# Kernel optimization log

Measured on AMD Instinct MI355X. Metric: run time of the kernel, lower is better.

Reference implementation:

```python
import jax, jax.numpy as jnp
import numpy as np

IN_DIM, UNITS, OUT_DIM = 128, 256, 8
DENSITY = 0.5  # 1 - sparsity_level
B, T = 256, 512


def _ncp_dims():
    Nm = OUT_DIM
    Nc = max(int(0.4 * (UNITS - Nm)), 1)   # command neurons (AutoNCP rule)
    Ni = UNITS - Nm - Nc                    # inter neurons
    return Ni, Nc, Nm


def _fanout_mask(rng, n_src, n_dst, fanout):
    # each source connects to `fanout` distinct random destinations
    idx = np.argsort(rng.random((n_src, n_dst)), axis=1)[:, :fanout]
    m = np.zeros((n_src, n_dst), dtype=np.int32)
    m[np.arange(n_src)[:, None], idx] = 1
    return m


def setup_inputs() -> dict:
    key = jax.random.key(0)
    rng = np.random.default_rng(22222)
    Ni, Nc, Nm = _ncp_dims()
    s_fan = max(int(Ni * DENSITY), 1)       # sensory fanout
    i_fan = max(int(Nc * DENSITY), 1)       # inter fanout
    m_fanin = max(int(Nc * DENSITY), 1)     # motor fanin
    M_si = _fanout_mask(rng, IN_DIM, Ni, s_fan)      # sensory -> inter
    M_ic = _fanout_mask(rng, Ni, Nc, i_fan)          # inter -> command
    M_cm = _fanout_mask(rng, Nm, Nc, m_fanin).T      # command -> motor (fanin per motor)

    def layer_mask(M_in, hid):
        # WiredCfCCell: concat input sparsity with dense ones for the recurrent block, then transpose
        return np.concatenate([M_in, np.ones((hid, hid), np.int32)], axis=0).T

    masks = [layer_mask(M_si, Ni), layer_mask(M_ic, Nc), layer_mask(M_cm, Nm)]
    dims = [(IN_DIM, Ni), (Ni, Nc), (Nc, Nm)]
    inp = {}
    for l, (fin, hid) in enumerate(dims):
        cat = fin + hid
        scale = 1.0 / np.sqrt(cat)
        for nm in ("w1", "w2", "wa", "wb"):
            inp[f"{nm}_{l}"] = jnp.asarray(rng.normal(0.0, scale, (hid, cat)).astype(np.float32))
        for nm in ("b1", "b2", "ba", "bb"):
            inp[f"{nm}_{l}"] = jnp.zeros((hid,), jnp.float32)
        inp[f"m{l}"] = jnp.asarray(masks[l])  # int32, constant sparsity mask
    k1, k2 = jax.random.split(key)
    inp["x"] = jax.random.normal(k1, (B, T, IN_DIM), jnp.float32)
    inp["dt"] = jax.random.uniform(k2, (1,), jnp.float32, 0.5, 1.5)
    return inp


def _cfc_cell(xh, w1, b1, w2, b2, wa, ba, wb, bb, m, ts):
    # CfCCell, mode='default', no backbone, sparsity mask on ff1/ff2 weights
    mf = m.astype(w1.dtype)
    ff1 = jnp.tanh(xh @ (w1 * mf).T + b1)
    ff2 = jnp.tanh(xh @ (w2 * mf).T + b2)
    t_interp = jax.nn.sigmoid((xh @ wa.T + ba) * ts + (xh @ wb.T + bb))
    return ff1 * (1.0 - t_interp) + t_interp * ff2


def _forward(x, dt, params, masks):
    Ni, Nc, Nm = _ncp_dims()
    ts = dt[0]
    h0 = jnp.zeros((x.shape[0], Ni), x.dtype)
    h1 = jnp.zeros((x.shape[0], Nc), x.dtype)
    h2 = jnp.zeros((x.shape[0], Nm), x.dtype)
    p0, p1, p2 = params

    def step(carry, xt):
        h0, h1, h2 = carry
        nh0 = _cfc_cell(jnp.concatenate([xt, h0], 1), *p0, masks[0], ts)
        nh1 = _cfc_cell(jnp.concatenate([nh0, h1], 1), *p1, masks[1], ts)
        nh2 = _cfc_cell(jnp.concatenate([nh1, h2], 1), *p2, masks[2], ts)
        return (nh0, nh1, nh2), nh2

    (h0, h1, h2), ys = jax.lax.scan(step, (h0, h1, h2), jnp.swapaxes(x, 0, 1))
    y = jnp.tanh(jnp.swapaxes(ys, 0, 1))          # (B, T, OUT_DIM), tanh output saturation
    h_out = jnp.concatenate([h0, h1, h2], axis=1)  # (B, units)
    return y, h_out


def reference(x, dt,
              w1_0, b1_0, w2_0, b2_0, wa_0, ba_0, wb_0, bb_0, m0,
              w1_1, b1_1, w2_1, b2_1, wa_1, ba_1, wb_1, bb_1, m1,
              w1_2, b1_2, w2_2, b2_2, wa_2, ba_2, wb_2, bb_2, m2):
    params = ((w1_0, b1_0, w2_0, b2_0, wa_0, ba_0, wb_0, bb_0),
              (w1_1, b1_1, w2_1, b2_1, wa_1, ba_1, wb_1, bb_1),
              (w1_2, b1_2, w2_2, b2_2, wa_2, ba_2, wb_2, bb_2))
    return _forward(x, dt, params, (m0, m1, m2))
```

## Files before the change

kernel.cpp:

```cpp
#include <hip/hip_runtime.h>
#include <cmath>


typedef _Float16 f16;
typedef f16 h4 __attribute__((ext_vector_type(4)));
typedef f16 h8 __attribute__((ext_vector_type(8)));
typedef float f4 __attribute__((ext_vector_type(4)));

#define MFMA(a, b, c) __builtin_amdgcn_mfma_f32_16x16x32_f16(a, b, c, 0, 0, 0)
#define RAW_BAR() asm volatile("s_waitcnt lgkmcnt(0)\n\ts_barrier" ::: "memory")

constexpr int IN_DIM = 128, Ni = 149, Nc = 99, Nm = 8;
constexpr int CAT0 = 277, CAT1 = 248, CAT2 = 107;
constexpr int Bsz = 256, Tsz = 512;
constexpr int TC = 128, NCH = 4, NBT = 16;
constexpr int NT0 = 30, NT1 = 21;
constexpr int S0 = 168, S2 = 136;
constexpr size_t XU0_HALVES = (size_t)TC * NBT * NT0 * 256;
constexpr size_t NH0_HALVES = (size_t)TC * NBT * 16 * 160;
constexpr size_t XU1_HALVES = (size_t)TC * NBT * NT1 * 256;
constexpr size_t H0S_HALVES = (size_t)NBT * 16 * S0;
constexpr size_t H12S_HALVES = (size_t)NBT * 2 * 16 * S2;
constexpr size_t YOFF = (size_t)Bsz * Tsz * 8;

constexpr int OFF_X0 = 0;
constexpr int OFF_R0 = 7680;
constexpr int OFF_X1 = 17280;
constexpr int OFF_R12A = 24000;
constexpr int OFF_R12B = 29376;
constexpr int NFRAG = 30144;

__device__ inline float rcpf_(float x) { return __builtin_amdgcn_rcpf(x); }
__device__ __forceinline__ float cfc_h(float a0, float a1, float a2) {
  float e0 = __expf(a0), e1 = __expf(a1), e2 = __expf(a2);
  float pa = 1.f + e0, ma = 1.f - e0;
  float pb = 1.f + e1, mb = 1.f - e1;
  float pc = 1.f + e2;
  float num = fmaf(ma * pb, e2, mb * pa);
  return num * rcpf_(pa * pb * pc);
}
__device__ __forceinline__ float tanhp_(float x) {
  float e = __expf(-2.f * x);
  return (1.f - e) * rcpf_(1.f + e);
}

__global__ __launch_bounds__(256) void pack_kernel(
    const float* __restrict__ w1_0, const float* __restrict__ w2_0,
    const float* __restrict__ wa_0, const float* __restrict__ wb_0,
    const int* __restrict__ m0,
    const float* __restrict__ w1_1, const float* __restrict__ w2_1,
    const float* __restrict__ wa_1, const float* __restrict__ wb_1,
    const int* __restrict__ m1,
    const float* __restrict__ w1_2, const float* __restrict__ w2_2,
    const float* __restrict__ wa_2, const float* __restrict__ wb_2,
    const int* __restrict__ m2, const float* __restrict__ dtp,
    f16* __restrict__ PK) {
  int idx = blockIdx.x * 256 + threadIdx.x;
  if (idx >= NFRAG) return;
  int lane = idx & 63, col = lane & 15, q = lane >> 4;
  float ts = dtp[0];
  const float* Wa = nullptr;
  const float* Wb = nullptr;
  const int* M = nullptr;
  int ld, n, nmax, k0, kmax;
  int mat;
  if (idx < OFF_R0) {
    int p = idx >> 6;
    mat = p / 40; int nt = (p >> 2) % 10, kt = p & 3;
    ld = CAT0; n = nt * 16 + col; nmax = Ni; k0 = kt * 32 + q * 8; kmax = IN_DIM;
    if (mat == 0) { Wa = w1_0; M = m0; }
    else if (mat == 1) { Wa = w2_0; M = m0; }
    else { Wa = wa_0; Wb = wb_0; }
  } else if (idx < OFF_X1) {
    int p = (idx - OFF_R0) >> 6;
    int g = p / 15; mat = (p / 5) % 3; int kt = p % 5;
    ld = CAT0; n = g * 16 + col; nmax = Ni; k0 = IN_DIM + kt * 32 + q * 8; kmax = CAT0;
    if (mat == 0) Wa = w1_0;
    else if (mat == 1) Wa = w2_0;
    else { Wa = wa_0; Wb = wb_0; }
  } else if (idx < OFF_R12A) {
    int p = (idx - OFF_X1) >> 6;
    mat = p / 35; int nt = (p / 5) % 7, kt = p % 5;
    ld = CAT1; n = nt * 16 + col; nmax = Nc; k0 = kt * 32 + q * 8; kmax = Ni;
    if (mat == 0) { Wa = w1_1; M = m1; }
    else if (mat == 1) { Wa = w2_1; M = m1; }
    else { Wa = wa_1; Wb = wb_1; }
  } else if (idx < OFF_R12B) {
    int p = (idx - OFF_R12A) >> 6;
    int wv = p / 12; mat = (p / 4) % 3; int kt = p & 3;
    ld = CAT1; n = wv * 16 + col; nmax = Nc; k0 = Ni + kt * 32 + q * 8; kmax = CAT1;
    if (mat == 0) Wa = w1_1;
    else if (mat == 1) Wa = w2_1;
    else { Wa = wa_1; Wb = wb_1; }
  } else {
    int p = (idx - OFF_R12B) >> 6;
    mat = p / 4; int kt = p & 3;
    ld = CAT2; n = col; nmax = Nm; k0 = kt * 32 + q * 8; kmax = CAT2;
    if (mat == 0) { Wa = w1_2; M = m2; }
    else if (mat == 1) { Wa = w2_2; M = m2; }
    else { Wa = wa_2; Wb = wb_2; }
  }
  h8 r;
#pragma unroll
  for (int j = 0; j < 8; j++) {
    int k = k0 + j;
    float v = 0.f;
    if (n < nmax && k < kmax) {
      if (mat < 2) {
        v = Wa[(size_t)n * ld + k];
        if (M) v *= (float)M[(size_t)n * ld + k];
        v *= -2.f;
      } else {
        v = -(ts * Wa[(size_t)n * ld + k] + Wb[(size_t)n * ld + k]);
      }
    }
    r[j] = (f16)v;
  }
  ((h8*)PK)[idx] = r;
}

__global__ __launch_bounds__(192, 2) void X_kernel(
    const h8* __restrict__ pk, const float* __restrict__ x,
    const f16* __restrict__ NH0, f16* __restrict__ XU0, f16* __restrict__ XU1,
    const float* __restrict__ b1_0, const float* __restrict__ b2_0,
    const float* __restrict__ ba_0, const float* __restrict__ bb_0,
    const float* __restrict__ b1_1, const float* __restrict__ b2_1,
    const float* __restrict__ ba_1, const float* __restrict__ bb_1,
    const float* __restrict__ dtp, int c) {
  __shared__ f16 stg[16 * 136];
  int tid = threadIdx.x;
  int w = tid >> 6, lane = tid & 63, col = lane & 15, q = lane >> 4;
  int wg = blockIdx.x;
  float ts = dtp[0];
  if (wg < 512) {
    if (c < 0) return;
    h8 Bf[7][5];
    float bias[7];
#pragma unroll
    for (int nt = 0; nt < 7; nt++) {
#pragma unroll
      for (int kt = 0; kt < 5; kt++)
        Bf[nt][kt] = pk[OFF_X1 + ((w * 7 + nt) * 5 + kt) * 64 + lane];
      int n = nt * 16 + col;
      bias[nt] = (n < Nc) ? (w == 0 ? -2.f * b1_1[n]
                                    : (w == 1 ? -2.f * b2_1[n]
                                              : -(ts * ba_1[n] + bb_1[n])))
                          : 0.f;
    }
    for (int i = 0; i < 4; i++) {
      int mt = wg * 4 + i;
      const f16* Ab = NH0 + (size_t)mt * 2560;
      h8 A[5];
#pragma unroll
      for (int kt = 0; kt < 5; kt++)
        A[kt] = *(const h8*)(Ab + col * 160 + kt * 32 + q * 8);
#pragma unroll
      for (int nt = 0; nt < 7; nt++) {
        float b = bias[nt];
        f4 acc = {b, b, b, b};
#pragma unroll
        for (int kt = 0; kt < 5; kt++) acc = MFMA(A[kt], Bf[nt][kt], acc);
        h4 o;
#pragma unroll
        for (int rr = 0; rr < 4; rr++) o[rr] = (f16)acc[rr];
        *(h4*)(XU1 + ((size_t)mt * NT1 + w * 7 + nt) * 256 + lane * 4) = o;
      }
    }
  } else {
    int cn = c + 1;
    if (cn >= NCH) return;
    int bx = wg - 512;
    h8 Bf[10][4];
    float bias[10];
#pragma unroll
    for (int nt = 0; nt < 10; nt++) {
#pragma unroll
      for (int kt = 0; kt < 4; kt++)
        Bf[nt][kt] = pk[OFF_X0 + ((w * 10 + nt) * 4 + kt) * 64 + lane];
      int n = nt * 16 + col;
      bias[nt] = (n < Ni) ? (w == 0 ? -2.f * b1_0[n]
                                    : (w == 1 ? -2.f * b2_0[n]
                                              : -(ts * ba_0[n] + bb_0[n])))
                          : 0.f;
    }
    for (int i = 0; i < 4; i++) {
      int mt = bx * 4 + i;
      int tl = mt >> 4, bt = mt & 15;
      int tg = cn * TC + tl;
      if (tid < 128) {
        int sr = tid >> 3, sc = (tid & 7) * 16;
        const float* xp = x + ((size_t)(bt * 16 + sr) * Tsz + tg) * IN_DIM + sc;
        h8 hv0, hv1;
#pragma unroll
        for (int j = 0; j < 8; j++) hv0[j] = (f16)xp[j];
#pragma unroll
        for (int j = 0; j < 8; j++) hv1[j] = (f16)xp[8 + j];
        *(h8*)(stg + sr * 136 + sc) = hv0;
        *(h8*)(stg + sr * 136 + sc + 8) = hv1;
      }
      __syncthreads();
      h8 A[4];
#pragma unroll
      for (int kt = 0; kt < 4; kt++)
        A[kt] = *(const h8*)(stg + col * 136 + kt * 32 + q * 8);
#pragma unroll
      for (int nt = 0; nt < 10; nt++) {
        float b = bias[nt];
        f4 acc = {b, b, b, b};
#pragma unroll
        for (int kt = 0; kt < 4; kt++) acc = MFMA(A[kt], Bf[nt][kt], acc);
        h4 o;
#pragma unroll
        for (int rr = 0; rr < 4; rr++) o[rr] = (f16)acc[rr];
        *(h4*)(XU0 + ((size_t)mt * NT0 + w * 10 + nt) * 256 + lane * 4) = o;
      }
      __syncthreads();
    }
  }
}

__device__ __forceinline__ void r0_step(
    const f16* br, f16* bw, const f16* __restrict__ XU0, f16* __restrict__ NH0,
    float* __restrict__ out, const h8 (&Bf)[3][5], h4 (&xu)[3],
    int t, int tload, int bt, int g, int lane, int col, int q, int n, bool last) {
  h8 A[5];
#pragma unroll
  for (int kt = 0; kt < 5; kt++)
    A[kt] = *(const h8*)(br + col * S0 + kt * 32 + q * 8);
  f4 acc0 = {(float)xu[0][0], (float)xu[0][1], (float)xu[0][2], (float)xu[0][3]};
  f4 acc1 = {(float)xu[1][0], (float)xu[1][1], (float)xu[1][2], (float)xu[1][3]};
  f4 acc2 = {(float)xu[2][0], (float)xu[2][1], (float)xu[2][2], (float)xu[2][3]};
  size_t mtl = (size_t)tload * NBT + bt;
#pragma unroll
  for (int mat = 0; mat < 3; mat++)
    xu[mat] = *(const h4*)(XU0 + (mtl * NT0 + mat * 10 + g) * 256 + lane * 4);
#pragma unroll
  for (int kt = 0; kt < 5; kt++) {
    acc0 = MFMA(A[kt], Bf[0][kt], acc0);
    acc1 = MFMA(A[kt], Bf[1][kt], acc1);
    acc2 = MFMA(A[kt], Bf[2][kt], acc2);
  }
  int mt = t * NBT + bt;
  f16* nh = NH0 + (size_t)mt * 2560;
#pragma unroll
  for (int r = 0; r < 4; r++) {
    int m = q * 4 + r;
    float h = cfc_h(acc0[r], acc1[r], acc2[r]);
    f16 h16 = (f16)h;
    bw[m * S0 + n] = h16;
    nh[m * 160 + n] = h16;
    if (last && n < Ni) out[YOFF + (size_t)(bt * 16 + m) * 256 + n] = h;
  }
}

__device__ __forceinline__ void r12l1_step(
    const f16* br, f16* bw, const f16* __restrict__ XU1, float* __restrict__ out,
    const h8 (&Bf)[3][4], h4 (&xu)[3],
    int tload, int bt, int w, int lane, int col, int q, int n, bool last) {
  h8 A[4];
#pragma unroll
  for (int kt = 0; kt < 4; kt++)
    A[kt] = *(const h8*)(br + col * S2 + kt * 32 + q * 8);
  f4 acc0 = {(float)xu[0][0], (float)xu[0][1], (float)xu[0][2], (float)xu[0][3]};
  f4 acc1 = {(float)xu[1][0], (float)xu[1][1], (float)xu[1][2], (float)xu[1][3]};
  f4 acc2 = {(float)xu[2][0], (float)xu[2][1], (float)xu[2][2], (float)xu[2][3]};
  size_t mtl = (size_t)tload * NBT + bt;
#pragma unroll
  for (int mat = 0; mat < 3; mat++)
    xu[mat] = *(const h4*)(XU1 + (mtl * NT1 + mat * 7 + w) * 256 + lane * 4);
#pragma unroll
  for (int kt = 0; kt < 4; kt++) {
    acc0 = MFMA(A[kt], Bf[0][kt], acc0);
    acc1 = MFMA(A[kt], Bf[1][kt], acc1);
    acc2 = MFMA(A[kt], Bf[2][kt], acc2);
  }
#pragma unroll
  for (int r = 0; r < 4; r++) {
    int m = q * 4 + r;
    float h = cfc_h(acc0[r], acc1[r], acc2[r]);
    if (n < Nc) {
      bw[m * S2 + n] = (f16)h;
      if (last) out[YOFF + (size_t)(bt * 16 + m) * 256 + Ni + n] = h;
    }
  }
}

__device__ __forceinline__ void r12l2_step(
    const f16* rb, f16* wb, float* __restrict__ out, const h8 (&Bf)[3][4],
    float bn0, float bn1, float bn2, int tg, int bt, int col, int q, bool last) {
  h8 A[4];
#pragma unroll
  for (int kt = 0; kt < 4; kt++)
    A[kt] = *(const h8*)(rb + col * S2 + kt * 32 + q * 8);
  f4 acc0 = {bn0, bn0, bn0, bn0};
  f4 acc1 = {bn1, bn1, bn1, bn1};
  f4 acc2 = {bn2, bn2, bn2, bn2};
#pragma unroll
  for (int kt = 0; kt < 4; kt++) {
    acc0 = MFMA(A[kt], Bf[0][kt], acc0);
    acc1 = MFMA(A[kt], Bf[1][kt], acc1);
    acc2 = MFMA(A[kt], Bf[2][kt], acc2);
  }
#pragma unroll
  for (int r = 0; r < 4; r++) {
    int m = q * 4 + r;
    float h = cfc_h(acc0[r], acc1[r], acc2[r]);
    if (col < Nm) {
      out[((size_t)(bt * 16 + m) * Tsz + tg) * 8 + col] = tanhp_(h);
      wb[m * S2 + Nc + col] = (f16)h;
      if (last) out[YOFF + (size_t)(bt * 16 + m) * 256 + Ni + Nc + col] = h;
    }
  }
}

__global__ __launch_bounds__(640) void R_kernel(
    const h8* __restrict__ pk,
    const float* __restrict__ c1, const float* __restrict__ c2,
    const float* __restrict__ ca, const float* __restrict__ cb,
    const float* __restrict__ dtp, const f16* __restrict__ XU0,
    const f16* __restrict__ XU1, f16* __restrict__ NH0,
    f16* __restrict__ H0S, f16* __restrict__ H12S, float* __restrict__ out, int c) {
  __shared__ __align__(16) char smem[2 * 16 * S0 * 2];
  int tid = threadIdx.x;
  int g = tid >> 6, lane = tid & 63, col = lane & 15, q = lane >> 4;
  int wg = blockIdx.x;

  if (wg < NBT) {
    if (c >= NCH) return;
    f16(*buf)[16 * S0] = (f16(*)[16 * S0])smem;
    int bt = wg;
    int n = g * 16 + col;
    h8 Bf[3][5];
#pragma unroll
    for (int mat = 0; mat < 3; mat++)
#pragma unroll
      for (int kt = 0; kt < 5; kt++)
        Bf[mat][kt] = pk[OFF_R0 + ((g * 3 + mat) * 5 + kt) * 64 + lane];

    for (int idx = tid; idx < 16 * S0; idx += 640) {
      buf[0][idx] = (c == 0) ? (f16)0.f : H0S[(size_t)bt * 16 * S0 + idx];
      buf[1][idx] = (f16)0.f;
    }
    __syncthreads();

    h4 xuA[3], xuB[3];
#pragma unroll
    for (int mat = 0; mat < 3; mat++) {
      xuA[mat] = *(const h4*)(XU0 + ((size_t)bt * NT0 + mat * 10 + g) * 256 + lane * 4);
      xuB[mat] =
          *(const h4*)(XU0 + ((size_t)(NBT + bt) * NT0 + mat * 10 + g) * 256 + lane * 4);
    }

    for (int t = 0; t < TC; t += 2) {
      bool lastA = (c == NCH - 1) && (t == TC - 1);
      int tlA = (t + 2 < TC) ? t + 2 : t;
      r0_step(buf[0], buf[1], XU0, NH0, out, Bf, xuA, t, tlA, bt, g, lane, col, q, n,
              lastA);
      RAW_BAR();
      bool lastB = (c == NCH - 1) && (t + 1 == TC - 1);
      int tlB = (t + 3 < TC) ? t + 3 : t + 1;
      r0_step(buf[1], buf[0], XU0, NH0, out, Bf, xuB, t + 1, tlB, bt, g, lane, col, q,
              n, lastB);
      RAW_BAR();
    }
    for (int idx = tid; idx < 16 * S0; idx += 640)
      H0S[(size_t)bt * 16 * S0 + idx] = buf[0][idx];

  } else {
    int cc = c - 1;
    if (cc < 0) return;
    f16(*buf)[16 * S2] = (f16(*)[16 * S2])smem;
    int bt = wg - NBT;
    int w = g;
    float ts = dtp[0];
    h8 Bf[3][4];
    float bn0 = 0.f, bn1 = 0.f, bn2 = 0.f;
    int n = w * 16 + col;
    if (w < 7) {
#pragma unroll
      for (int mat = 0; mat < 3; mat++)
#pragma unroll
        for (int kt = 0; kt < 4; kt++)
          Bf[mat][kt] = pk[OFF_R12A + ((w * 3 + mat) * 4 + kt) * 64 + lane];
    } else if (w == 7) {
#pragma unroll
      for (int mat = 0; mat < 3; mat++)
#pragma unroll
        for (int kt = 0; kt < 4; kt++)
          Bf[mat][kt] = pk[OFF_R12B + (mat * 4 + kt) * 64 + lane];
      bn0 = (col < Nm) ? -2.f * c1[col] : 0.f;
      bn1 = (col < Nm) ? -2.f * c2[col] : 0.f;
      bn2 = (col < Nm) ? -(ts * ca[col] + cb[col]) : 0.f;
    }
    for (int idx = tid; idx < 2 * 16 * S2; idx += 640)
      ((f16*)buf)[idx] = (cc == 0) ? (f16)0.f : H12S[(size_t)bt * 2 * 16 * S2 + idx];
    __syncthreads();

    h4 xuA[3], xuB[3];
    if (w < 7) {
#pragma unroll
      for (int mat = 0; mat < 3; mat++) {
        xuA[mat] =
            *(const h4*)(XU1 + ((size_t)bt * NT1 + mat * 7 + w) * 256 + lane * 4);
        xuB[mat] = *(const h4*)(XU1 +
                                ((size_t)(NBT + bt) * NT1 + mat * 7 + w) * 256 +
                                lane * 4);
      }
    }

    for (int t = 0; t < TC; t += 2) {
      if (w < 7) {
        int tlA = (t + 2 < TC) ? t + 2 : t;
        bool lastA = (cc == NCH - 1) && (t == TC - 1);
        r12l1_step(buf[0], buf[1], XU1, out, Bf, xuA, tlA, bt, w, lane, col, q, n,
                   lastA);
      }
      RAW_BAR();
      if (w == 7)
        r12l2_step(buf[1], buf[0], out, Bf, bn0, bn1, bn2, cc * TC + t, bt, col, q,
                   false);
      if (w < 7) {
        int tlB = (t + 3 < TC) ? t + 3 : t + 1;
        bool lastB = (cc == NCH - 1) && (t + 1 == TC - 1);
        r12l1_step(buf[1], buf[0], XU1, out, Bf, xuB, tlB, bt, w, lane, col, q, n,
                   lastB);
      }
      RAW_BAR();
      if (w == 7)
        r12l2_step(buf[0], buf[1], out, Bf, bn0, bn1, bn2, cc * TC + t + 1, bt, col, q,
                   (cc == NCH - 1) && (t + 1 == TC - 1));
    }
    __syncthreads();
    for (int idx = tid; idx < 2 * 16 * S2; idx += 640)
      H12S[(size_t)bt * 2 * 16 * S2 + idx] = ((f16*)buf)[idx];
  }
}

extern "C" void kernel_launch(void* const* d_in, const int* in_sizes, int n_in,
                              void* d_out, int out_size, void* d_ws, size_t ws_size,
                              hipStream_t stream) {
  const float* w1_0 = (const float*)d_in[0];
  const float* w2_0 = (const float*)d_in[1];
  const float* wa_0 = (const float*)d_in[2];
  const float* wb_0 = (const float*)d_in[3];
  const float* b1_0 = (const float*)d_in[4];
  const float* b2_0 = (const float*)d_in[5];
  const float* ba_0 = (const float*)d_in[6];
  const float* bb_0 = (const float*)d_in[7];
  const int* m0 = (const int*)d_in[8];
  const float* w1_1 = (const float*)d_in[9];
  const float* w2_1 = (const float*)d_in[10];
  const float* wa_1 = (const float*)d_in[11];
  const float* wb_1 = (const float*)d_in[12];
  const float* b1_1 = (const float*)d_in[13];
  const float* b2_1 = (const float*)d_in[14];
  const float* ba_1 = (const float*)d_in[15];
  const float* bb_1 = (const float*)d_in[16];
  const int* m1 = (const int*)d_in[17];
  const float* w1_2 = (const float*)d_in[18];
  const float* w2_2 = (const float*)d_in[19];
  const float* wa_2 = (const float*)d_in[20];
  const float* wb_2 = (const float*)d_in[21];
  const float* c1 = (const float*)d_in[22];
  const float* c2 = (const float*)d_in[23];
  const float* ca = (const float*)d_in[24];
  const float* cb = (const float*)d_in[25];
  const int* m2 = (const int*)d_in[26];
  const float* x = (const float*)d_in[27];
  const float* dt = (const float*)d_in[28];
  float* out = (float*)d_out;

  f16* XU0 = (f16*)d_ws;
  f16* NH0 = XU0 + XU0_HALVES;
  f16* XU1 = NH0 + NH0_HALVES;
  f16* H0S = XU1 + XU1_HALVES;
  f16* H12S = H0S + H0S_HALVES;
  f16* PK = H12S + H12S_HALVES;
  const h8* pk = (const h8*)PK;

  pack_kernel<<<(NFRAG + 255) / 256, 256, 0, stream>>>(
      w1_0, w2_0, wa_0, wb_0, m0, w1_1, w2_1, wa_1, wb_1, m1,
      w1_2, w2_2, wa_2, wb_2, m2, dt, PK);

  X_kernel<<<1024, 192, 0, stream>>>(pk, x, NH0, XU0, XU1, b1_0, b2_0, ba_0, bb_0,
                                     b1_1, b2_1, ba_1, bb_1, dt, -1);

  for (int c = 0; c <= NCH; c++) {
    R_kernel<<<32, 640, 0, stream>>>(pk, c1, c2, ca, cb, dt, XU0, XU1, NH0, H0S,
                                     H12S, out, c);
    if (c < NCH)
      X_kernel<<<1024, 192, 0, stream>>>(pk, x, NH0, XU0, XU1, b1_0, b2_0, ba_0,
                                         bb_0, b1_1, b2_1, ba_1, bb_1, dt, c);
  }
}
```

Baseline: 828.4 us.

## Fuse input projection into recurrent kernel and compute layer-1 input on the fly

Removes the separate X_kernel launches. The layer-0 input projection now runs on extra workgroups inside R_kernel, concurrently with the recurrences, using double-buffered XU0 and NH0 chunks. The layer-1 input projection is no longer precomputed into XU1: the layer-1 waves multiply directly against NH0 tiles that are staged into LDS by two extra prefetch waves. The chunk size is halved to 64 timesteps, which doubles the number of chunks and launches. This trades extra MFMA work on the serial recurrent critical path for fewer launches, less memory traffic and overlap of the projection with the recurrence.

```diff
diff --git a/kernel.cpp b/kernel.cpp
--- a/kernel.cpp
+++ b/kernel.cpp
@@ -13,12 +13,12 @@
 constexpr int IN_DIM = 128, Ni = 149, Nc = 99, Nm = 8;
 constexpr int CAT0 = 277, CAT1 = 248, CAT2 = 107;
 constexpr int Bsz = 256, Tsz = 512;
-constexpr int TC = 128, NCH = 4, NBT = 16;
-constexpr int NT0 = 30, NT1 = 21;
+constexpr int TC = 64, NCH = 8, NBT = 16;
+constexpr int NT0 = 30;
 constexpr int S0 = 168, S2 = 136;
-constexpr size_t XU0_HALVES = (size_t)TC * NBT * NT0 * 256;
-constexpr size_t NH0_HALVES = (size_t)TC * NBT * 16 * 160;
-constexpr size_t XU1_HALVES = (size_t)TC * NBT * NT1 * 256;
+constexpr int NXWG = 128;
+constexpr size_t XU0C = (size_t)TC * NBT * NT0 * 256;
+constexpr size_t NH0C = (size_t)TC * NBT * 2560;
 constexpr size_t H0S_HALVES = (size_t)NBT * 16 * S0;
 constexpr size_t H12S_HALVES = (size_t)NBT * 2 * 16 * S2;
 constexpr size_t YOFF = (size_t)Bsz * Tsz * 8;
@@ -119,106 +119,6 @@
   ((h8*)PK)[idx] = r;
 }
 
-__global__ __launch_bounds__(192, 2) void X_kernel(
-    const h8* __restrict__ pk, const float* __restrict__ x,
-    const f16* __restrict__ NH0, f16* __restrict__ XU0, f16* __restrict__ XU1,
-    const float* __restrict__ b1_0, const float* __restrict__ b2_0,
-    const float* __restrict__ ba_0, const float* __restrict__ bb_0,
-    const float* __restrict__ b1_1, const float* __restrict__ b2_1,
-    const float* __restrict__ ba_1, const float* __restrict__ bb_1,
-    const float* __restrict__ dtp, int c) {
-  __shared__ f16 stg[16 * 136];
-  int tid = threadIdx.x;
-  int w = tid >> 6, lane = tid & 63, col = lane & 15, q = lane >> 4;
-  int wg = blockIdx.x;
-  float ts = dtp[0];
-  if (wg < 512) {
-    if (c < 0) return;
-    h8 Bf[7][5];
-    float bias[7];
-#pragma unroll
-    for (int nt = 0; nt < 7; nt++) {
-#pragma unroll
-      for (int kt = 0; kt < 5; kt++)
-        Bf[nt][kt] = pk[OFF_X1 + ((w * 7 + nt) * 5 + kt) * 64 + lane];
-      int n = nt * 16 + col;
-      bias[nt] = (n < Nc) ? (w == 0 ? -2.f * b1_1[n]
-                                    : (w == 1 ? -2.f * b2_1[n]
-                                              : -(ts * ba_1[n] + bb_1[n])))
-                          : 0.f;
-    }
-    for (int i = 0; i < 4; i++) {
-      int mt = wg * 4 + i;
-      const f16* Ab = NH0 + (size_t)mt * 2560;
-      h8 A[5];
-#pragma unroll
-      for (int kt = 0; kt < 5; kt++)
-        A[kt] = *(const h8*)(Ab + col * 160 + kt * 32 + q * 8);
-#pragma unroll
-      for (int nt = 0; nt < 7; nt++) {
-        float b = bias[nt];
-        f4 acc = {b, b, b, b};
-#pragma unroll
-        for (int kt = 0; kt < 5; kt++) acc = MFMA(A[kt], Bf[nt][kt], acc);
-        h4 o;
-#pragma unroll
-        for (int rr = 0; rr < 4; rr++) o[rr] = (f16)acc[rr];
-        *(h4*)(XU1 + ((size_t)mt * NT1 + w * 7 + nt) * 256 + lane * 4) = o;
-      }
-    }
-  } else {
-    int cn = c + 1;
-    if (cn >= NCH) return;
-    int bx = wg - 512;
-    h8 Bf[10][4];
-    float bias[10];
-#pragma unroll
-    for (int nt = 0; nt < 10; nt++) {
-#pragma unroll
-      for (int kt = 0; kt < 4; kt++)
-        Bf[nt][kt] = pk[OFF_X0 + ((w * 10 + nt) * 4 + kt) * 64 + lane];
-      int n = nt * 16 + col;
-      bias[nt] = (n < Ni) ? (w == 0 ? -2.f * b1_0[n]
-                                    : (w == 1 ? -2.f * b2_0[n]
-                                              : -(ts * ba_0[n] + bb_0[n])))
-                          : 0.f;
-    }
-    for (int i = 0; i < 4; i++) {
-      int mt = bx * 4 + i;
-      int tl = mt >> 4, bt = mt & 15;
-      int tg = cn * TC + tl;
-      if (tid < 128) {
-        int sr = tid >> 3, sc = (tid & 7) * 16;
-        const float* xp = x + ((size_t)(bt * 16 + sr) * Tsz + tg) * IN_DIM + sc;
-        h8 hv0, hv1;
-#pragma unroll
-        for (int j = 0; j < 8; j++) hv0[j] = (f16)xp[j];
-#pragma unroll
-        for (int j = 0; j < 8; j++) hv1[j] = (f16)xp[8 + j];
-        *(h8*)(stg + sr * 136 + sc) = hv0;
-        *(h8*)(stg + sr * 136 + sc + 8) = hv1;
-      }
-      __syncthreads();
-      h8 A[4];
-#pragma unroll
-      for (int kt = 0; kt < 4; kt++)
-        A[kt] = *(const h8*)(stg + col * 136 + kt * 32 + q * 8);
-#pragma unroll
-      for (int nt = 0; nt < 10; nt++) {
-        float b = bias[nt];
-        f4 acc = {b, b, b, b};
-#pragma unroll
-        for (int kt = 0; kt < 4; kt++) acc = MFMA(A[kt], Bf[nt][kt], acc);
-        h4 o;
-#pragma unroll
-        for (int rr = 0; rr < 4; rr++) o[rr] = (f16)acc[rr];
-        *(h4*)(XU0 + ((size_t)mt * NT0 + w * 10 + nt) * 256 + lane * 4) = o;
-      }
-      __syncthreads();
-    }
-  }
-}
-
 __device__ __forceinline__ void r0_step(
     const f16* br, f16* bw, const f16* __restrict__ XU0, f16* __restrict__ NH0,
     float* __restrict__ out, const h8 (&Bf)[3][5], h4 (&xu)[3],
@@ -254,25 +154,26 @@
 }
 
 __device__ __forceinline__ void r12l1_step(
-    const f16* br, f16* bw, const f16* __restrict__ XU1, float* __restrict__ out,
-    const h8 (&Bf)[3][4], h4 (&xu)[3],
-    int tload, int bt, int w, int lane, int col, int q, int n, bool last) {
-  h8 A[4];
-#pragma unroll
-  for (int kt = 0; kt < 4; kt++)
-    A[kt] = *(const h8*)(br + col * S2 + kt * 32 + q * 8);
-  f4 acc0 = {(float)xu[0][0], (float)xu[0][1], (float)xu[0][2], (float)xu[0][3]};
-  f4 acc1 = {(float)xu[1][0], (float)xu[1][1], (float)xu[1][2], (float)xu[1][3]};
-  f4 acc2 = {(float)xu[2][0], (float)xu[2][1], (float)xu[2][2], (float)xu[2][3]};
-  size_t mtl = (size_t)tload * NBT + bt;
-#pragma unroll
-  for (int mat = 0; mat < 3; mat++)
-    xu[mat] = *(const h4*)(XU1 + (mtl * NT1 + mat * 7 + w) * 256 + lane * 4);
+    const f16* brN, const f16* br, f16* bw, float* __restrict__ out,
+    const h8 (&BfI)[3][5], const h8 (&BfR)[3][4],
+    float bn0, float bn1, float bn2,
+    int bt, int col, int q, int n, bool last) {
+  f4 acc0 = {bn0, bn0, bn0, bn0};
+  f4 acc1 = {bn1, bn1, bn1, bn1};
+  f4 acc2 = {bn2, bn2, bn2, bn2};
+#pragma unroll
+  for (int kt = 0; kt < 5; kt++) {
+    h8 A = *(const h8*)(brN + col * S0 + kt * 32 + q * 8);
+    acc0 = MFMA(A, BfI[0][kt], acc0);
+    acc1 = MFMA(A, BfI[1][kt], acc1);
+    acc2 = MFMA(A, BfI[2][kt], acc2);
+  }
 #pragma unroll
   for (int kt = 0; kt < 4; kt++) {
-    acc0 = MFMA(A[kt], Bf[0][kt], acc0);
-    acc1 = MFMA(A[kt], Bf[1][kt], acc1);
-    acc2 = MFMA(A[kt], Bf[2][kt], acc2);
+    h8 A = *(const h8*)(br + col * S2 + kt * 32 + q * 8);
+    acc0 = MFMA(A, BfR[0][kt], acc0);
+    acc1 = MFMA(A, BfR[1][kt], acc1);
+    acc2 = MFMA(A, BfR[2][kt], acc2);
   }
 #pragma unroll
   for (int r = 0; r < 4; r++) {
@@ -315,18 +216,26 @@
 
 __global__ __launch_bounds__(640) void R_kernel(
     const h8* __restrict__ pk,
+    const float* __restrict__ b1_0, const float* __restrict__ b2_0,
+    const float* __restrict__ ba_0, const float* __restrict__ bb_0,
+    const float* __restrict__ b1_1, const float* __restrict__ b2_1,
+    const float* __restrict__ ba_1, const float* __restrict__ bb_1,
     const float* __restrict__ c1, const float* __restrict__ c2,
     const float* __restrict__ ca, const float* __restrict__ cb,
-    const float* __restrict__ dtp, const f16* __restrict__ XU0,
-    const f16* __restrict__ XU1, f16* __restrict__ NH0,
-    f16* __restrict__ H0S, f16* __restrict__ H12S, float* __restrict__ out, int c) {
-  __shared__ __align__(16) char smem[2 * 16 * S0 * 2];
+    const float* __restrict__ dtp, const float* __restrict__ x,
+    f16* __restrict__ XU0, f16* __restrict__ NH0,
+    f16* __restrict__ H0S, f16* __restrict__ H12S,
+    float* __restrict__ out, int c) {
+  __shared__ __align__(16) char smem[19456];
   int tid = threadIdx.x;
   int g = tid >> 6, lane = tid & 63, col = lane & 15, q = lane >> 4;
   int wg = blockIdx.x;
+  float ts = dtp[0];
 
   if (wg < NBT) {
-    if (c >= NCH) return;
+    if (c < 0 || c >= NCH) return;
+    const f16* XU0r = XU0 + (size_t)(c & 1) * XU0C;
+    f16* NH0w = NH0 + (size_t)(c & 1) * NH0C;
     f16(*buf)[16 * S0] = (f16(*)[16 * S0])smem;
     int bt = wg;
     int n = g * 16 + col;
@@ -346,93 +255,172 @@
     h4 xuA[3], xuB[3];
 #pragma unroll
     for (int mat = 0; mat < 3; mat++) {
-      xuA[mat] = *(const h4*)(XU0 + ((size_t)bt * NT0 + mat * 10 + g) * 256 + lane * 4);
-      xuB[mat] =
-          *(const h4*)(XU0 + ((size_t)(NBT + bt) * NT0 + mat * 10 + g) * 256 + lane * 4);
+      xuA[mat] = *(const h4*)(XU0r + ((size_t)bt * NT0 + mat * 10 + g) * 256 + lane * 4);
+      xuB[mat] = *(const h4*)(XU0r +
+                              ((size_t)(NBT + bt) * NT0 + mat * 10 + g) * 256 + lane * 4);
     }
 
     for (int t = 0; t < TC; t += 2) {
-      bool lastA = (c == NCH - 1) && (t == TC - 1);
       int tlA = (t + 2 < TC) ? t + 2 : t;
-      r0_step(buf[0], buf[1], XU0, NH0, out, Bf, xuA, t, tlA, bt, g, lane, col, q, n,
-              lastA);
+      r0_step(buf[0], buf[1], XU0r, NH0w, out, Bf, xuA, t, tlA, bt, g, lane, col, q, n,
+              false);
       RAW_BAR();
       bool lastB = (c == NCH - 1) && (t + 1 == TC - 1);
       int tlB = (t + 3 < TC) ? t + 3 : t + 1;
-      r0_step(buf[1], buf[0], XU0, NH0, out, Bf, xuB, t + 1, tlB, bt, g, lane, col, q,
+      r0_step(buf[1], buf[0], XU0r, NH0w, out, Bf, xuB, t + 1, tlB, bt, g, lane, col, q,
               n, lastB);
       RAW_BAR();
     }
     for (int idx = tid; idx < 16 * S0; idx += 640)
       H0S[(size_t)bt * 16 * S0 + idx] = buf[0][idx];
 
-  } else {
+  } else if (wg < 2 * NBT) {
     int cc = c - 1;
-    if (cc < 0) return;
+    if (cc < 0 || cc >= NCH) return;
+    const f16* NH0r = NH0 + (size_t)(cc & 1) * NH0C;
     f16(*buf)[16 * S2] = (f16(*)[16 * S2])smem;
+    f16* bufN0 = (f16*)(smem + 2 * 16 * S2 * 2);
+    f16* bufN1 = bufN0 + 16 * S0;
     int bt = wg - NBT;
     int w = g;
-    float ts = dtp[0];
-    h8 Bf[3][4];
+    int n = w * 16 + col;
+    h8 BfI[3][5], BfR[3][4], Bf2[3][4];
     float bn0 = 0.f, bn1 = 0.f, bn2 = 0.f;
-    int n = w * 16 + col;
     if (w < 7) {
 #pragma unroll
+      for (int mat = 0; mat < 3; mat++) {
+#pragma unroll
+        for (int kt = 0; kt < 5; kt++)
+          BfI[mat][kt] = pk[OFF_X1 + (mat * 35 + w * 5 + kt) * 64 + lane];
+#pragma unroll
+        for (int kt = 0; kt < 4; kt++)
+          BfR[mat][kt] = pk[OFF_R12A + ((w * 3 + mat) * 4 + kt) * 64 + lane];
+      }
+      bn0 = (n < Nc) ? -2.f * b1_1[n] : 0.f;
+      bn1 = (n < Nc) ? -2.f * b2_1[n] : 0.f;
+      bn2 = (n < Nc) ? -(ts * ba_1[n] + bb_1[n]) : 0.f;
+    } else if (w == 7) {
+#pragma unroll
       for (int mat = 0; mat < 3; mat++)
 #pragma unroll
         for (int kt = 0; kt < 4; kt++)
-          Bf[mat][kt] = pk[OFF_R12A + ((w * 3 + mat) * 4 + kt) * 64 + lane];
-    } else if (w == 7) {
-#pragma unroll
-      for (int mat = 0; mat < 3; mat++)
-#pragma unroll
-        for (int kt = 0; kt < 4; kt++)
-          Bf[mat][kt] = pk[OFF_R12B + (mat * 4 + kt) * 64 + lane];
+          Bf2[mat][kt] = pk[OFF_R12B + (mat * 4 + kt) * 64 + lane];
       bn0 = (col < Nm) ? -2.f * c1[col] : 0.f;
       bn1 = (col < Nm) ? -2.f * c2[col] : 0.f;
       bn2 = (col < Nm) ? -(ts * ca[col] + cb[col]) : 0.f;
     }
+    int offG[3] = {0, 0, 0}, offL[3] = {0, 0, 0};
+    bool vj[3] = {false, false, false};
+    h8 sreg[3];
+    if (w >= 8) {
+      int half = w - 8;
+#pragma unroll
+      for (int j = 0; j < 3; j++) {
+        int idx = j * 64 + lane;
+        vj[j] = idx < 160;
+        int rr = vj[j] ? idx / 20 : 0, seg = vj[j] ? idx % 20 : 0;
+        int row = half * 8 + rr;
+        offG[j] = row * 160 + seg * 8;
+        offL[j] = row * S0 + seg * 8;
+      }
+      const f16* base = NH0r + (size_t)bt * 2560;
+#pragma unroll
+      for (int j = 0; j < 3; j++) if (vj[j]) sreg[j] = *(const h8*)(base + offG[j]);
+#pragma unroll
+      for (int j = 0; j < 3; j++) if (vj[j]) *(h8*)(bufN0 + offL[j]) = sreg[j];
+      base = NH0r + ((size_t)NBT + bt) * 2560;
+#pragma unroll
+      for (int j = 0; j < 3; j++) if (vj[j]) sreg[j] = *(const h8*)(base + offG[j]);
+    }
     for (int idx = tid; idx < 2 * 16 * S2; idx += 640)
       ((f16*)buf)[idx] = (cc == 0) ? (f16)0.f : H12S[(size_t)bt * 2 * 16 * S2 + idx];
     __syncthreads();
 
-    h4 xuA[3], xuB[3];
-    if (w < 7) {
-#pragma unroll
-      for (int mat = 0; mat < 3; mat++) {
-        xuA[mat] =
-            *(const h4*)(XU1 + ((size_t)bt * NT1 + mat * 7 + w) * 256 + lane * 4);
-        xuB[mat] = *(const h4*)(XU1 +
-                                ((size_t)(NBT + bt) * NT1 + mat * 7 + w) * 256 +
-                                lane * 4);
-      }
-    }
-
     for (int t = 0; t < TC; t += 2) {
       if (w < 7) {
-        int tlA = (t + 2 < TC) ? t + 2 : t;
-        bool lastA = (cc == NCH - 1) && (t == TC - 1);
-        r12l1_step(buf[0], buf[1], XU1, out, Bf, xuA, tlA, bt, w, lane, col, q, n,
-                   lastA);
+        r12l1_step(bufN0, buf[0], buf[1], out, BfI, BfR, bn0, bn1, bn2, bt, col, q, n,
+                   false);
+      } else if (w >= 8) {
+#pragma unroll
+        for (int j = 0; j < 3; j++) if (vj[j]) *(h8*)(bufN1 + offL[j]) = sreg[j];
+        int tl = (t + 2 < TC) ? t + 2 : TC - 1;
+        const f16* base = NH0r + ((size_t)tl * NBT + bt) * 2560;
+#pragma unroll
+        for (int j = 0; j < 3; j++) if (vj[j]) sreg[j] = *(const h8*)(base + offG[j]);
       }
       RAW_BAR();
       if (w == 7)
-        r12l2_step(buf[1], buf[0], out, Bf, bn0, bn1, bn2, cc * TC + t, bt, col, q,
+        r12l2_step(buf[1], buf[0], out, Bf2, bn0, bn1, bn2, cc * TC + t, bt, col, q,
                    false);
       if (w < 7) {
-        int tlB = (t + 3 < TC) ? t + 3 : t + 1;
         bool lastB = (cc == NCH - 1) && (t + 1 == TC - 1);
-        r12l1_step(buf[1], buf[0], XU1, out, Bf, xuB, tlB, bt, w, lane, col, q, n,
+        r12l1_step(bufN1, buf[1], buf[0], out, BfI, BfR, bn0, bn1, bn2, bt, col, q, n,
                    lastB);
+      } else if (w >= 8) {
+#pragma unroll
+        for (int j = 0; j < 3; j++) if (vj[j]) *(h8*)(bufN0 + offL[j]) = sreg[j];
+        int tl = (t + 3 < TC) ? t + 3 : TC - 1;
+        const f16* base = NH0r + ((size_t)tl * NBT + bt) * 2560;
+#pragma unroll
+        for (int j = 0; j < 3; j++) if (vj[j]) sreg[j] = *(const h8*)(base + offG[j]);
       }
       RAW_BAR();
       if (w == 7)
-        r12l2_step(buf[0], buf[1], out, Bf, bn0, bn1, bn2, cc * TC + t + 1, bt, col, q,
+        r12l2_step(buf[0], buf[1], out, Bf2, bn0, bn1, bn2, cc * TC + t + 1, bt, col, q,
                    (cc == NCH - 1) && (t + 1 == TC - 1));
     }
     __syncthreads();
     for (int idx = tid; idx < 2 * 16 * S2; idx += 640)
       H12S[(size_t)bt * 2 * 16 * S2 + idx] = ((f16*)buf)[idx];
+
+  } else {
+    int cn = c + 1;
+    if (cn >= NCH) return;
+    f16* XU0w = XU0 + (size_t)(cn & 1) * XU0C;
+    f16* stg = (f16*)smem;
+    int bx = wg - 2 * NBT;
+    int w = g;
+    int n = w * 16 + col;
+    h8 Bx[3][4];
+    float bias[3];
+#pragma unroll
+    for (int mat = 0; mat < 3; mat++)
+#pragma unroll
+      for (int kt = 0; kt < 4; kt++)
+        Bx[mat][kt] = pk[OFF_X0 + ((mat * 10 + w) * 4 + kt) * 64 + lane];
+    bias[0] = (n < Ni) ? -2.f * b1_0[n] : 0.f;
+    bias[1] = (n < Ni) ? -2.f * b2_0[n] : 0.f;
+    bias[2] = (n < Ni) ? -(ts * ba_0[n] + bb_0[n]) : 0.f;
+    for (int i = 0; i < (TC * NBT) / NXWG; i++) {
+      int mt = bx * ((TC * NBT) / NXWG) + i;
+      int tl = mt >> 4, bt = mt & 15;
+      int tg = cn * TC + tl;
+      if (tid < 256) {
+        int sr = tid >> 4, sc = (tid & 15) * 8;
+        const float* xp = x + ((size_t)(bt * 16 + sr) * Tsz + tg) * IN_DIM + sc;
+        h8 hv;
+#pragma unroll
+        for (int j = 0; j < 8; j++) hv[j] = (f16)xp[j];
+        *(h8*)(stg + sr * 136 + sc) = hv;
+      }
+      __syncthreads();
+      h8 A[4];
+#pragma unroll
+      for (int kt = 0; kt < 4; kt++)
+        A[kt] = *(const h8*)(stg + col * 136 + kt * 32 + q * 8);
+#pragma unroll
+      for (int mat = 0; mat < 3; mat++) {
+        float b = bias[mat];
+        f4 acc = {b, b, b, b};
+#pragma unroll
+        for (int kt = 0; kt < 4; kt++) acc = MFMA(A[kt], Bx[mat][kt], acc);
+        h4 o;
+#pragma unroll
+        for (int rr = 0; rr < 4; rr++) o[rr] = (f16)acc[rr];
+        *(h4*)(XU0w + ((size_t)mt * NT0 + mat * 10 + w) * 256 + lane * 4) = o;
+      }
+      __syncthreads();
+    }
   }
 }
 
@@ -471,9 +459,8 @@
   float* out = (float*)d_out;
 
   f16* XU0 = (f16*)d_ws;
-  f16* NH0 = XU0 + XU0_HALVES;
-  f16* XU1 = NH0 + NH0_HALVES;
-  f16* H0S = XU1 + XU1_HALVES;
+  f16* NH0 = XU0 + 2 * XU0C;
+  f16* H0S = NH0 + 2 * NH0C;
   f16* H12S = H0S + H0S_HALVES;
   f16* PK = H12S + H12S_HALVES;
   const h8* pk = (const h8*)PK;
@@ -482,14 +469,8 @@
       w1_0, w2_0, wa_0, wb_0, m0, w1_1, w2_1, wa_1, wb_1, m1,
       w1_2, w2_2, wa_2, wb_2, m2, dt, PK);
 
-  X_kernel<<<1024, 192, 0, stream>>>(pk, x, NH0, XU0, XU1, b1_0, b2_0, ba_0, bb_0,
-                                     b1_1, b2_1, ba_1, bb_1, dt, -1);
-
-  for (int c = 0; c <= NCH; c++) {
-    R_kernel<<<32, 640, 0, stream>>>(pk, c1, c2, ca, cb, dt, XU0, XU1, NH0, H0S,
-                                     H12S, out, c);
-    if (c < NCH)
-      X_kernel<<<1024, 192, 0, stream>>>(pk, x, NH0, XU0, XU1, b1_0, b2_0, ba_0,
-                                         bb_0, b1_1, b2_1, ba_1, bb_1, dt, c);
-  }
-}
+  for (int c = -1; c <= NCH; c++)
+    R_kernel<<<2 * NBT + NXWG, 640, 0, stream>>>(
+        pk, b1_0, b2_0, ba_0, bb_0, b1_1, b2_1, ba_1, bb_1,
+        c1, c2, ca, cb, dt, x, XU0, NH0, H0S, H12S, out, c);
+}
```

Measured after the change: 1.456 ms. 75.7% more time.
